# Performance work log

Measured on AMD Instinct MI355X. Metric: run time of the kernel, lower is better.

Reference implementation:

```python
import jax, jax.numpy as jnp
import numpy as np

B, L, K = 4, 1024, 48
EF, NF, NPE, NRBF, NCLS = 128, 128, 16, 16, 3
MAXREL = 32
EDGE_IN = NPE + NRBF * 25  # 416


def setup_inputs():
    key = jax.random.key(0)
    ks = jax.random.split(key, 8)
    X = jax.random.normal(ks[0], (B, L, 4, 3), jnp.float32)
    mask = jnp.ones((B, L), jnp.float32)
    R_idx = jnp.arange(B * L, dtype=jnp.int64).reshape(B, L)
    chain_labels = jax.random.randint(ks[1], (B, L), 0, 4).astype(jnp.int64)
    membrane_per_residue_labels = jax.random.randint(ks[2], (B, L), 0, NCLS).astype(jnp.int64)
    pe_w = jax.random.normal(ks[3], (2 * MAXREL + 2, NPE), jnp.float32) * 0.05
    pe_b = jax.random.normal(ks[4], (NPE,), jnp.float32) * 0.05
    edge_w = jax.random.normal(ks[5], (EDGE_IN, EF), jnp.float32) * 0.05
    ne_g = jnp.ones((EF,), jnp.float32)
    ne_b = jnp.zeros((EF,), jnp.float32)
    node_w = jax.random.normal(ks[6], (NCLS, NF), jnp.float32) * 0.05
    nn_g = jnp.ones((NF,), jnp.float32)
    nn_b = jnp.zeros((NF,), jnp.float32)
    return {"X": X, "mask": mask, "R_idx": R_idx, "chain_labels": chain_labels,
            "membrane_per_residue_labels": membrane_per_residue_labels,
            "pe_w": pe_w, "pe_b": pe_b, "edge_w": edge_w, "ne_g": ne_g, "ne_b": ne_b,
            "node_w": node_w, "nn_g": nn_g, "nn_b": nn_b}


def _rbf(D):
    mu = jnp.linspace(2.0, 22.0, NRBF)
    sigma = (22.0 - 2.0) / NRBF
    return jnp.exp(-(((D[..., None] - mu) / sigma) ** 2))


def _gather_nb(v, e_idx):
    # v: [B, L, ...] -> [B, L, K, ...] gathered along residue dim
    return jax.vmap(lambda vi, ii: vi[ii])(v, e_idx)


def _ln(x, g, b, eps=1e-5):
    mu = jnp.mean(x, -1, keepdims=True)
    var = jnp.mean((x - mu) ** 2, -1, keepdims=True)
    return (x - mu) / jnp.sqrt(var + eps) * g + b


# 24 atom-pair RBFs after the Ca-Ca (D_neighbors) one, in the original concat order
PAIRS = [("N","N"),("C","C"),("O","O"),("Cb","Cb"),("Ca","N"),("Ca","C"),("Ca","O"),
         ("Ca","Cb"),("N","C"),("N","O"),("N","Cb"),("Cb","C"),("Cb","O"),("O","C"),
         ("N","Ca"),("C","Ca"),("O","Ca"),("Cb","Ca"),("C","N"),("O","N"),("Cb","N"),
         ("C","Cb"),("O","Cb"),("C","O")]


def reference(X, mask, R_idx, chain_labels, membrane_per_residue_labels,
              pe_w, pe_b, edge_w, ne_g, ne_b, node_w, nn_g, nn_b):
    Na, Ca, Cc, Oo = X[:, :, 0], X[:, :, 1], X[:, :, 2], X[:, :, 3]
    bvec = Ca - Na
    cvec = Cc - Ca
    avec = jnp.cross(bvec, cvec)
    Cb = -0.58273431 * avec + 0.56802827 * bvec - 0.54067466 * cvec + Ca
    coords = {"N": Na, "Ca": Ca, "C": Cc, "O": Oo, "Cb": Cb}

    # masked Ca-Ca distances + kNN (single NxN pass)
    mask2 = mask[:, :, None] * mask[:, None, :]
    dX = Ca[:, :, None, :] - Ca[:, None, :, :]
    D = mask2 * jnp.sqrt(jnp.sum(dX ** 2, -1) + 1e-6)
    D_max = jnp.max(D, -1, keepdims=True)
    D_adj = D + (1.0 - mask2) * D_max
    negD, E_idx = jax.lax.top_k(-D_adj, K)
    D_neighbors = -negD  # [B, L, K]

    # gather neighbor coords once, compute the 25 RBF features on N*K pairs only
    nb = {n: _gather_nb(v, E_idx) for n, v in coords.items()}  # [B, L, K, 3]
    rbf_list = [_rbf(D_neighbors)]
    for an, bn in PAIRS:
        d = jnp.sqrt(jnp.sum((coords[an][:, :, None, :] - nb[bn]) ** 2, -1) + 1e-6)
        rbf_list.append(_rbf(d))
    RBF_all = jnp.concatenate(rbf_list, -1)  # [B, L, K, 400]

    # positional encodings on gathered offsets / chain equality
    off = R_idx[:, :, None] - _gather_nb(R_idx, E_idx)           # [B, L, K]
    E_chains = (chain_labels[:, :, None] == _gather_nb(chain_labels, E_idx)).astype(jnp.int32)
    d = jnp.clip(off + MAXREL, 0, 2 * MAXREL).astype(jnp.int32) * E_chains + (1 - E_chains) * (2 * MAXREL + 1)
    d1h = jax.nn.one_hot(d, 2 * MAXREL + 2, dtype=jnp.float32)
    E_pos = d1h @ pe_w + pe_b                                     # [B, L, K, 16]

    E = jnp.concatenate([E_pos, RBF_all], -1) @ edge_w            # [B, L, K, 128]
    E = _ln(E, ne_g, ne_b)

    C1h = jax.nn.one_hot(membrane_per_residue_labels, NCLS, dtype=jnp.float32)
    V = _ln(C1h @ node_w, nn_g, nn_b)                             # [B, L, 128]
    return V, E, E_idx
```

## Files before the change

kernel.cpp:

```cpp
#include <hip/hip_runtime.h>
#include <math.h>

#define B_ 4
#define L_ 1024
#define K_ 48
#define EF_ 128
#define NF_ 128
#define NPE_ 16
#define NRBF_ 16
#define MAXREL_ 32
#define EDGE_IN_ 416

#define V_SIZE   (B_*L_*NF_)
#define E_OFF    (V_SIZE)
#define E_SIZE   (B_*L_*K_*EF_)
#define EIDX_OFF (E_OFF + E_SIZE)

#define XH_STRIDE 232
#define SE_STRIDE 132

typedef __attribute__((ext_vector_type(8))) short bf16x8;
typedef __attribute__((ext_vector_type(4))) float f32x4;
typedef __attribute__((ext_vector_type(4))) unsigned u32x4;

__device__ const int PA_[25] = {1, 0,2,3,4, 1,1,1,1, 0,0,0, 4,4, 3, 0,2,3,4, 2,3,4, 2,3, 2};
__device__ const int PB_[25] = {1, 0,2,3,4, 0,2,3,4, 2,3,4, 2,3, 2, 1,1,1,1, 0,0,0, 4,4, 3};

__device__ __forceinline__ unsigned short f2bf(float f){
    unsigned u = __float_as_uint(f);
    unsigned r = u + 0x7fffu + ((u >> 16) & 1u);
    return (unsigned short)(r >> 16);
}

__global__ __launch_bounds__(256) void wprep_kernel(const float* __restrict__ w,
                                                    unsigned short* __restrict__ wt)
{
    int idx = blockIdx.x * 256 + threadIdx.x;
    if (idx >= EDGE_IN_ * EF_) return;
    int f = idx & 127;
    int k = idx >> 7;
    wt[f * EDGE_IN_ + k] = f2bf(w[k * EF_ + f]);
}

__global__ __launch_bounds__(128) void v_kernel(const int* __restrict__ labels,
                                                const float* __restrict__ node_w,
                                                const float* __restrict__ g,
                                                const float* __restrict__ bb,
                                                float* __restrict__ out)
{
    int gi = blockIdx.x;
    int f  = threadIdx.x;
    int lbl = labels[gi];
    float v = node_w[lbl*NF_ + f];

    __shared__ float red[2];
    __shared__ float red2[2];
    float s = v;
    #pragma unroll
    for (int m = 1; m < 64; m <<= 1) s += __shfl_xor(s, m, 64);
    if ((f & 63) == 0) red[f >> 6] = s;
    __syncthreads();
    float mu = (red[0] + red[1]) * (1.0f / NF_);
    float d = v - mu;
    float s2 = d * d;
    #pragma unroll
    for (int m = 1; m < 64; m <<= 1) s2 += __shfl_xor(s2, m, 64);
    if ((f & 63) == 0) red2[f >> 6] = s2;
    __syncthreads();
    float var = (red2[0] + red2[1]) * (1.0f / NF_);
    out[gi*NF_ + f] = d * rsqrtf(var + 1e-5f) * g[f] + bb[f];
}

__global__ __launch_bounds__(256, 5) void fused_kernel(const float* __restrict__ X,
                                                   const float* __restrict__ mask,
                                                   const int* __restrict__ Ridx,
                                                   const int* __restrict__ chains,
                                                   const float* __restrict__ pe_w,
                                                   const float* __restrict__ pe_b,
                                                   const unsigned short* __restrict__ wt,
                                                   const float* __restrict__ ne_g,
                                                   const float* __restrict__ ne_b,
                                                   float* __restrict__ out)
{
    __shared__ __align__(16) unsigned char sBuf[K_ * SE_STRIDE * 4];
    float* sCa = (float*)sBuf;
    float* sM  = (float*)(sBuf + 12288);
    unsigned short* xh = (unsigned short*)sBuf;
    float* sE = (float*)sBuf;

    __shared__ float sAI[16];
    __shared__ float sAJ[K_][16];
    __shared__ int   sJ[K_];
    __shared__ int   sDpos[K_];
    __shared__ unsigned hist[256];
    __shared__ float wmax[4];
    __shared__ int sSelBin;
    __shared__ unsigned sSelLo, sSelCnt;
    __shared__ unsigned long long sTkey;
    __shared__ unsigned long long cand[K_];
    __shared__ unsigned sCnt;

    int tid = threadIdx.x;
    int gi  = blockIdx.x;
    int b   = gi >> 10;
    int i   = gi & (L_ - 1);

    for (int idx = tid; idx < L_ * 3; idx += 256) {
        int j = idx / 3, d = idx - j * 3;
        sCa[idx] = X[(((size_t)((b << 10) + j)) * 4 + 1) * 3 + d];
    }
    for (int j = tid; j < L_; j += 256) sM[j] = mask[(b << 10) + j];
    if (tid == 0) sCnt = 0;
    __syncthreads();

    float cx = sCa[i*3+0], cy = sCa[i*3+1], cz = sCa[i*3+2];
    float mi = sM[i];

    float lmax = 0.0f;
    #pragma unroll
    for (int q = 0; q < 4; ++q) {
        int j = tid + q * 256;
        float dx = cx - sCa[j*3+0];
        float dy = cy - sCa[j*3+1];
        float dz = cz - sCa[j*3+2];
        float dist = sqrtf(dx*dx + dy*dy + dz*dz + 1e-6f);
        lmax = fmaxf(lmax, mi * sM[j] * dist);
    }
    #pragma unroll
    for (int m = 1; m < 64; m <<= 1) lmax = fmaxf(lmax, __shfl_xor(lmax, m, 64));
    if ((tid & 63) == 0) wmax[tid >> 6] = lmax;
    __syncthreads();
    float Dmax = fmaxf(fmaxf(wmax[0], wmax[1]), fmaxf(wmax[2], wmax[3]));

    unsigned long long key[4];
    bool act[4];
    #pragma unroll
    for (int q = 0; q < 4; ++q) {
        int j = tid + q * 256;
        float dx = cx - sCa[j*3+0];
        float dy = cy - sCa[j*3+1];
        float dz = cz - sCa[j*3+2];
        float dist = sqrtf(dx*dx + dy*dy + dz*dz + 1e-6f);
        float m2 = mi * sM[j];
        float Dadj = m2 * dist + (1.0f - m2) * Dmax;
        key[q] = (((unsigned long long)__float_as_uint(Dadj)) << 32) | (unsigned)j;
        act[q] = true;
    }

    unsigned r = K_ - 1;
    unsigned long long T = 0;
    const int shifts[6] = {56, 48, 40, 32, 8, 0};
    #pragma unroll 1
    for (int p = 0; p < 6; ++p) {
        int sh = shifts[p];
        hist[tid] = 0;
        __syncthreads();
        #pragma unroll
        for (int q = 0; q < 4; ++q)
            if (act[q]) atomicAdd(&hist[(unsigned)((key[q] >> sh) & 255ULL)], 1u);
        __syncthreads();
        if (tid < 64) {
            unsigned b0 = hist[tid*4+0], b1 = hist[tid*4+1], b2 = hist[tid*4+2], b3 = hist[tid*4+3];
            unsigned s0 = b0, s1 = s0 + b1, s2 = s1 + b2, s3 = s2 + b3;
            unsigned s = s3;
            #pragma unroll
            for (int m = 1; m < 64; m <<= 1) {
                unsigned o = __shfl_up(s, m, 64);
                if (tid >= m) s += o;
            }
            unsigned base = s - s3;
            hist[tid*4+0] = base + s0;
            hist[tid*4+1] = base + s1;
            hist[tid*4+2] = base + s2;
            hist[tid*4+3] = base + s3;
        }
        __syncthreads();
        unsigned lo = (tid == 0) ? 0u : hist[tid - 1];
        unsigned hi = hist[tid];
        if (r >= lo && r < hi) { sSelBin = tid; sSelLo = lo; sSelCnt = hi - lo; }
        __syncthreads();
        int bsel = sSelBin;
        r -= sSelLo;
        T |= ((unsigned long long)(unsigned)bsel) << sh;
        #pragma unroll
        for (int q = 0; q < 4; ++q)
            act[q] = act[q] && ((unsigned)((key[q] >> sh) & 255ULL) == (unsigned)bsel);
        if (sSelCnt == 1) {
            #pragma unroll
            for (int q = 0; q < 4; ++q)
                if (act[q]) sTkey = key[q];
            __syncthreads();
            T = sTkey;
            break;
        }
        __syncthreads();
    }

    #pragma unroll
    for (int q = 0; q < 4; ++q)
        if (key[q] <= T) {
            unsigned pos = atomicAdd(&sCnt, 1u);
            cand[pos] = key[q];
        }
    __syncthreads();

    if (tid < 64) {
        unsigned long long k64 = (tid < K_) ? cand[tid] : 0xffffffffffffffffULL;
        #pragma unroll
        for (unsigned kk = 2; kk <= 64; kk <<= 1) {
            #pragma unroll
            for (unsigned jj = kk >> 1; jj > 0; jj >>= 1) {
                unsigned long long o = __shfl_xor(k64, jj, 64);
                bool lower = (tid & jj) == 0;
                bool asc   = (tid & kk) == 0;
                unsigned long long mn = (k64 < o) ? k64 : o;
                unsigned long long mx = (k64 < o) ? o : k64;
                k64 = (lower == asc) ? mn : mx;
            }
        }
        if (tid < K_) {
            int j = (int)(unsigned)(k64 & 0xffffffffULL);
            sJ[tid] = j;
            out[EIDX_OFF + (size_t)gi * K_ + tid] = (float)j;
        }
    }
    __syncthreads();

    if (tid < K_ + 1) {
        int rr = (tid < K_) ? sJ[tid] : i;
        const float* xr = X + ((size_t)((b << 10) + rr)) * 12;
        float n0=xr[0],  n1=xr[1],  n2=xr[2];
        float a0=xr[3],  a1=xr[4],  a2=xr[5];
        float c0=xr[6],  c1=xr[7],  c2=xr[8];
        float o0=xr[9],  o1=xr[10], o2=xr[11];
        float bx=a0-n0, by=a1-n1, bz=a2-n2;
        float vx=c0-a0, vy=c1-a1, vz=c2-a2;
        float ax = by*vz - bz*vy;
        float ay = bz*vx - bx*vz;
        float az = bx*vy - by*vx;
        float cb0 = -0.58273431f*ax + 0.56802827f*bx - 0.54067466f*vx + a0;
        float cb1 = -0.58273431f*ay + 0.56802827f*by - 0.54067466f*vy + a1;
        float cb2 = -0.58273431f*az + 0.56802827f*bz - 0.54067466f*vz + a2;
        float* dst = (tid < K_) ? &sAJ[tid][0] : &sAI[0];
        dst[0]=n0;  dst[1]=n1;  dst[2]=n2;
        dst[3]=a0;  dst[4]=a1;  dst[5]=a2;
        dst[6]=c0;  dst[7]=c1;  dst[8]=c2;
        dst[9]=o0;  dst[10]=o1; dst[11]=o2;
        dst[12]=cb0; dst[13]=cb1; dst[14]=cb2;
    }
    if (tid >= 64 && tid < 64 + K_) {
        int e = tid - 64;
        int j = sJ[e];
        int off  = Ridx[gi] - Ridx[(b << 10) + j];
        int same = (chains[gi] == chains[(b << 10) + j]);
        int dcl = off + MAXREL_;
        dcl = dcl < 0 ? 0 : (dcl > 2*MAXREL_ ? 2*MAXREL_ : dcl);
        sDpos[e] = same ? dcl : (2*MAXREL_ + 1);
    }
    __syncthreads();

    const int wv = tid >> 6;
    const int ln = tid & 63;
    const int lr = ln & 15;
    const int lg = ln >> 4;

    f32x4 acc[3][2];
    #pragma unroll
    for (int rf = 0; rf < 3; ++rf)
        #pragma unroll
        for (int cf = 0; cf < 2; ++cf)
            acc[rf][cf] = (f32x4){0.0f, 0.0f, 0.0f, 0.0f};

    const unsigned short* wbase0 = wt + (size_t)(wv*32 + lr) * EDGE_IN_ + lg*8;
    const unsigned short* wbase1 = wt + (size_t)(wv*32 + 16 + lr) * EDGE_IN_ + lg*8;

    #pragma unroll
    for (int h = 0; h < 2; ++h) {
        if (h == 0) {
            #pragma unroll
            for (int p = 0; p < 2; ++p) {
                int idx = tid + p * 256;
                if (idx < 384) {
                    int e = idx >> 3, cc = (idx & 7) * 2;
                    int dp = sDpos[e];
                    float v0 = pe_w[dp*NPE_ + cc]     + pe_b[cc];
                    float v1 = pe_w[dp*NPE_ + cc + 1] + pe_b[cc + 1];
                    unsigned pk;
                    asm("v_cvt_pk_bf16_f32 %0, %1, %2" : "=v"(pk) : "v"(v0), "v"(v1));
                    *(unsigned*)&xh[e * XH_STRIDE + cc] = pk;
                }
            }
            #pragma unroll
            for (int p = 0; p < 3; ++p) {
                int idx = tid + p * 256;
                if (idx < 624) {
                    int e = idx / 13, g2 = idx - e * 13;
                    float dx = sAI[PA_[g2]*3+0] - sAJ[e][PB_[g2]*3+0];
                    float dy = sAI[PA_[g2]*3+1] - sAJ[e][PB_[g2]*3+1];
                    float dz = sAI[PA_[g2]*3+2] - sAJ[e][PB_[g2]*3+2];
                    float dist = sqrtf(dx*dx + dy*dy + dz*dz + 1e-6f);
                    float t = 0.8f * dist - 1.6f;
                    unsigned pk[8];
                    #pragma unroll
                    for (int rr = 0; rr < 8; ++rr) {
                        float v0 = __expf(-t * t); t -= 1.06666672f;
                        float v1 = __expf(-t * t); t -= 1.06666672f;
                        asm("v_cvt_pk_bf16_f32 %0, %1, %2" : "=v"(pk[rr]) : "v"(v0), "v"(v1));
                    }
                    u32x4 w0 = {pk[0], pk[1], pk[2], pk[3]};
                    u32x4 w1 = {pk[4], pk[5], pk[6], pk[7]};
                    int cb = NPE_ + g2 * 16;
                    *(u32x4*)&xh[e * XH_STRIDE + cb]     = w0;
                    *(u32x4*)&xh[e * XH_STRIDE + cb + 8] = w1;
                }
            }
        } else {
            #pragma unroll
            for (int p = 0; p < 3; ++p) {
                int idx = tid + p * 256;
                if (idx < 576) {
                    int e = idx / 12, g2 = 13 + (idx - e * 12);
                    float dx = sAI[PA_[g2]*3+0] - sAJ[e][PB_[g2]*3+0];
                    float dy = sAI[PA_[g2]*3+1] - sAJ[e][PB_[g2]*3+1];
                    float dz = sAI[PA_[g2]*3+2] - sAJ[e][PB_[g2]*3+2];
                    float dist = sqrtf(dx*dx + dy*dy + dz*dz + 1e-6f);
                    float t = 0.8f * dist - 1.6f;
                    unsigned pk[8];
                    #pragma unroll
                    for (int rr = 0; rr < 8; ++rr) {
                        float v0 = __expf(-t * t); t -= 1.06666672f;
                        float v1 = __expf(-t * t); t -= 1.06666672f;
                        asm("v_cvt_pk_bf16_f32 %0, %1, %2" : "=v"(pk[rr]) : "v"(v0), "v"(v1));
                    }
                    u32x4 w0 = {pk[0], pk[1], pk[2], pk[3]};
                    u32x4 w1 = {pk[4], pk[5], pk[6], pk[7]};
                    int cb = (g2 - 13) * 16;
                    *(u32x4*)&xh[e * XH_STRIDE + cb]     = w0;
                    *(u32x4*)&xh[e * XH_STRIDE + cb + 8] = w1;
                }
            }
        }
        __syncthreads();

        const int kb  = h ? 224 : 0;
        const int nks = h ? 6 : 7;
        #pragma unroll 4
        for (int ks = 0; ks < nks; ++ks) {
            int k0 = ks * 32;
            bf16x8 a[3], bh[2];
            bh[0] = *(const bf16x8*)(wbase0 + kb + k0);
            bh[1] = *(const bf16x8*)(wbase1 + kb + k0);
            #pragma unroll
            for (int rf = 0; rf < 3; ++rf)
                a[rf] = *(const bf16x8*)&xh[(rf*16 + lr) * XH_STRIDE + k0 + lg*8];
            #pragma unroll
            for (int rf = 0; rf < 3; ++rf) {
                #pragma unroll
                for (int cf = 0; cf < 2; ++cf)
                    acc[rf][cf] = __builtin_amdgcn_mfma_f32_16x16x32_bf16(a[rf], bh[cf], acc[rf][cf], 0, 0, 0);
            }
        }
        __syncthreads();
    }

    #pragma unroll
    for (int rf = 0; rf < 3; ++rf)
        #pragma unroll
        for (int cf = 0; cf < 2; ++cf)
            #pragma unroll
            for (int r4 = 0; r4 < 4; ++r4) {
                int row = rf*16 + lg*4 + r4;
                int col = wv*32 + cf*16 + lr;
                sE[row * SE_STRIDE + col] = acc[rf][cf][r4];
            }
    __syncthreads();

    int l16 = tid & 15;
    float gv[8], bv[8];
    #pragma unroll
    for (int q = 0; q < 8; ++q) { gv[q] = ne_g[l16*8 + q]; bv[q] = ne_b[l16*8 + q]; }

    for (int p = 0; p < 3; ++p) {
        int e = p*16 + (tid >> 4);
        float vals[8];
        #pragma unroll
        for (int q = 0; q < 8; ++q) vals[q] = sE[e * SE_STRIDE + l16*8 + q];
        float sum = 0.0f;
        #pragma unroll
        for (int q = 0; q < 8; ++q) sum += vals[q];
        #pragma unroll
        for (int m = 1; m < 16; m <<= 1) sum += __shfl_xor(sum, m, 64);
        float mu = sum * (1.0f / 128.0f);
        float s2 = 0.0f;
        #pragma unroll
        for (int q = 0; q < 8; ++q) { float d = vals[q] - mu; s2 += d * d; }
        #pragma unroll
        for (int m = 1; m < 16; m <<= 1) s2 += __shfl_xor(s2, m, 64);
        float rstd = rsqrtf(s2 * (1.0f / 128.0f) + 1e-5f);

        float* dst = out + E_OFF + (size_t)(gi * K_ + e) * EF_ + l16*8;
        f32x4 o0, o1;
        o0[0] = (vals[0] - mu) * rstd * gv[0] + bv[0];
        o0[1] = (vals[1] - mu) * rstd * gv[1] + bv[1];
        o0[2] = (vals[2] - mu) * rstd * gv[2] + bv[2];
        o0[3] = (vals[3] - mu) * rstd * gv[3] + bv[3];
        o1[0] = (vals[4] - mu) * rstd * gv[4] + bv[4];
        o1[1] = (vals[5] - mu) * rstd * gv[5] + bv[5];
        o1[2] = (vals[6] - mu) * rstd * gv[6] + bv[6];
        o1[3] = (vals[7] - mu) * rstd * gv[7] + bv[7];
        __builtin_nontemporal_store(o0, (f32x4*)dst);
        __builtin_nontemporal_store(o1, (f32x4*)(dst + 4));
    }
}

extern "C" void kernel_launch(void* const* d_in, const int* in_sizes, int n_in,
                              void* d_out, int out_size, void* d_ws, size_t ws_size,
                              hipStream_t stream)
{
    const float* X      = (const float*)d_in[0];
    const float* mask   = (const float*)d_in[1];
    const int*   Ridx   = (const int*)d_in[2];
    const int*   chains = (const int*)d_in[3];
    const int*   memb   = (const int*)d_in[4];
    const float* pe_w   = (const float*)d_in[5];
    const float* pe_b   = (const float*)d_in[6];
    const float* edge_w = (const float*)d_in[7];
    const float* ne_g   = (const float*)d_in[8];
    const float* ne_b   = (const float*)d_in[9];
    const float* node_w = (const float*)d_in[10];
    const float* nn_g   = (const float*)d_in[11];
    const float* nn_b   = (const float*)d_in[12];
    float* out = (float*)d_out;

    unsigned short* wt = (unsigned short*)d_ws;

    wprep_kernel<<<(EDGE_IN_*EF_ + 255)/256, 256, 0, stream>>>(edge_w, wt);
    v_kernel<<<B_*L_, 128, 0, stream>>>(memb, node_w, nn_g, nn_b, out);
    fused_kernel<<<B_*L_, 256, 0, stream>>>(X, mask, Ridx, chains, pe_w, pe_b,
                                            wt, ne_g, ne_b, out);
}
```

Before: 97.85 us.

## Shrink LDS via quarter-sized feature staging and register-side LayerNorm

The bf16 feature tile is built and consumed in four K-chunks with a 136-element stride instead of two halves, so the shared buffer shrinks to 16KB. Scratch arrays are overlaid in one aux buffer, and launch bounds are raised to 7 blocks per SM. LayerNorm now runs straight from the MFMA accumulators using per-wave partial sums and a one-pass variance, with no fp32 staging of E in shared memory. The radix-select early exit is dropped and the first distance pass is reused. Costs: more barriers, scalar (non-vectorised) output stores, and a one-pass variance that is less numerically robust.

```diff
diff --git a/kernel.cpp b/kernel.cpp
--- a/kernel.cpp
+++ b/kernel.cpp
@@ -16,8 +16,7 @@
 #define E_SIZE   (B_*L_*K_*EF_)
 #define EIDX_OFF (E_OFF + E_SIZE)
 
-#define XH_STRIDE 232
-#define SE_STRIDE 132
+#define XH4_STRIDE 136
 
 typedef __attribute__((ext_vector_type(8))) short bf16x8;
 typedef __attribute__((ext_vector_type(4))) float f32x4;
@@ -30,6 +29,59 @@
     unsigned u = __float_as_uint(f);
     unsigned r = u + 0x7fffu + ((u >> 16) & 1u);
     return (unsigned short)(r >> 16);
+}
+
+__device__ __forceinline__ float pair_dist(const float* sAI, const float (*sAJ)[16], int e, int g2) {
+    float dx = sAI[PA_[g2]*3+0] - sAJ[e][PB_[g2]*3+0];
+    float dy = sAI[PA_[g2]*3+1] - sAJ[e][PB_[g2]*3+1];
+    float dz = sAI[PA_[g2]*3+2] - sAJ[e][PB_[g2]*3+2];
+    return sqrtf(dx*dx + dy*dy + dz*dz + 1e-6f);
+}
+
+__device__ __forceinline__ void rbf16(unsigned short* dst, float dist) {
+    float t = 0.8f * dist - 1.6f;
+    unsigned pk[8];
+    #pragma unroll
+    for (int rr = 0; rr < 8; ++rr) {
+        float v0 = __expf(-t * t); t -= 1.06666672f;
+        float v1 = __expf(-t * t); t -= 1.06666672f;
+        asm("v_cvt_pk_bf16_f32 %0, %1, %2" : "=v"(pk[rr]) : "v"(v0), "v"(v1));
+    }
+    u32x4 w0 = {pk[0], pk[1], pk[2], pk[3]};
+    u32x4 w1 = {pk[4], pk[5], pk[6], pk[7]};
+    *(u32x4*)dst = w0;
+    *(u32x4*)(dst + 8) = w1;
+}
+
+template<int NG, int GF, int CB>
+__device__ __forceinline__ void rbf_quarter(unsigned short* xh, const float* sAI,
+                                            const float (*sAJ)[16], int tid) {
+    for (int idx = tid; idx < K_ * NG; idx += 256) {
+        int e = idx / NG, g = idx - e * NG;
+        rbf16(&xh[e * XH4_STRIDE + CB + g * 16], pair_dist(sAI, sAJ, e, GF + g));
+    }
+}
+
+template<int NKS, int KB>
+__device__ __forceinline__ void mfma_quarter(f32x4 (&acc)[3][2], const unsigned short* xh,
+                                             const unsigned short* w0p, const unsigned short* w1p,
+                                             int lr, int lg) {
+    #pragma unroll
+    for (int ks = 0; ks < NKS; ++ks) {
+        int k0 = ks * 32;
+        bf16x8 a0, a1, a2, wb0, wb1;
+        wb0 = *(const bf16x8*)(w0p + KB + k0);
+        wb1 = *(const bf16x8*)(w1p + KB + k0);
+        a0 = *(const bf16x8*)&xh[(lr)      * XH4_STRIDE + k0 + lg*8];
+        a1 = *(const bf16x8*)&xh[(16 + lr) * XH4_STRIDE + k0 + lg*8];
+        a2 = *(const bf16x8*)&xh[(32 + lr) * XH4_STRIDE + k0 + lg*8];
+        acc[0][0] = __builtin_amdgcn_mfma_f32_16x16x32_bf16(a0, wb0, acc[0][0], 0, 0, 0);
+        acc[0][1] = __builtin_amdgcn_mfma_f32_16x16x32_bf16(a0, wb1, acc[0][1], 0, 0, 0);
+        acc[1][0] = __builtin_amdgcn_mfma_f32_16x16x32_bf16(a1, wb0, acc[1][0], 0, 0, 0);
+        acc[1][1] = __builtin_amdgcn_mfma_f32_16x16x32_bf16(a1, wb1, acc[1][1], 0, 0, 0);
+        acc[2][0] = __builtin_amdgcn_mfma_f32_16x16x32_bf16(a2, wb0, acc[2][0], 0, 0, 0);
+        acc[2][1] = __builtin_amdgcn_mfma_f32_16x16x32_bf16(a2, wb1, acc[2][1], 0, 0, 0);
+    }
 }
 
 __global__ __launch_bounds__(256) void wprep_kernel(const float* __restrict__ w,
@@ -71,7 +123,7 @@
     out[gi*NF_ + f] = d * rsqrtf(var + 1e-5f) * g[f] + bb[f];
 }
 
-__global__ __launch_bounds__(256, 5) void fused_kernel(const float* __restrict__ X,
+__global__ __launch_bounds__(256, 7) void fused_kernel(const float* __restrict__ X,
                                                    const float* __restrict__ mask,
                                                    const int* __restrict__ Ridx,
                                                    const int* __restrict__ chains,
@@ -82,23 +134,25 @@
                                                    const float* __restrict__ ne_b,
                                                    float* __restrict__ out)
 {
-    __shared__ __align__(16) unsigned char sBuf[K_ * SE_STRIDE * 4];
-    float* sCa = (float*)sBuf;
-    float* sM  = (float*)(sBuf + 12288);
-    unsigned short* xh = (unsigned short*)sBuf;
-    float* sE = (float*)sBuf;
-
+    __shared__ __align__(16) unsigned char sBuf[16384];
+    __shared__ __align__(16) unsigned char sAux[1536];
     __shared__ float sAI[16];
     __shared__ float sAJ[K_][16];
     __shared__ int   sJ[K_];
     __shared__ int   sDpos[K_];
-    __shared__ unsigned hist[256];
-    __shared__ float wmax[4];
-    __shared__ int sSelBin;
-    __shared__ unsigned sSelLo, sSelCnt;
-    __shared__ unsigned long long sTkey;
-    __shared__ unsigned long long cand[K_];
-    __shared__ unsigned sCnt;
+
+    float* sCa = (float*)sBuf;
+    float* sM  = (float*)(sBuf + 12288);
+    unsigned short* xh = (unsigned short*)sBuf;
+
+    unsigned long long* cand = (unsigned long long*)sAux;
+    unsigned* hist   = (unsigned*)(sAux + 384);
+    float*    wmax   = (float*)(sAux + 1408);
+    int*      sSelBin= (int*)(sAux + 1424);
+    unsigned* sSelLo = (unsigned*)(sAux + 1428);
+    unsigned* sCnt   = (unsigned*)(sAux + 1432);
+    float* stats  = (float*)sAux;
+    float* stats2 = (float*)(sAux + 768);
 
     int tid = threadIdx.x;
     int gi  = blockIdx.x;
@@ -110,30 +164,14 @@
         sCa[idx] = X[(((size_t)((b << 10) + j)) * 4 + 1) * 3 + d];
     }
     for (int j = tid; j < L_; j += 256) sM[j] = mask[(b << 10) + j];
-    if (tid == 0) sCnt = 0;
+    if (tid == 0) *sCnt = 0;
     __syncthreads();
 
     float cx = sCa[i*3+0], cy = sCa[i*3+1], cz = sCa[i*3+2];
     float mi = sM[i];
 
+    float dist4[4], m2r[4];
     float lmax = 0.0f;
-    #pragma unroll
-    for (int q = 0; q < 4; ++q) {
-        int j = tid + q * 256;
-        float dx = cx - sCa[j*3+0];
-        float dy = cy - sCa[j*3+1];
-        float dz = cz - sCa[j*3+2];
-        float dist = sqrtf(dx*dx + dy*dy + dz*dz + 1e-6f);
-        lmax = fmaxf(lmax, mi * sM[j] * dist);
-    }
-    #pragma unroll
-    for (int m = 1; m < 64; m <<= 1) lmax = fmaxf(lmax, __shfl_xor(lmax, m, 64));
-    if ((tid & 63) == 0) wmax[tid >> 6] = lmax;
-    __syncthreads();
-    float Dmax = fmaxf(fmaxf(wmax[0], wmax[1]), fmaxf(wmax[2], wmax[3]));
-
-    unsigned long long key[4];
-    bool act[4];
     #pragma unroll
     for (int q = 0; q < 4; ++q) {
         int j = tid + q * 256;
@@ -142,7 +180,21 @@
         float dz = cz - sCa[j*3+2];
         float dist = sqrtf(dx*dx + dy*dy + dz*dz + 1e-6f);
         float m2 = mi * sM[j];
-        float Dadj = m2 * dist + (1.0f - m2) * Dmax;
+        dist4[q] = dist; m2r[q] = m2;
+        lmax = fmaxf(lmax, m2 * dist);
+    }
+    #pragma unroll
+    for (int m = 1; m < 64; m <<= 1) lmax = fmaxf(lmax, __shfl_xor(lmax, m, 64));
+    if ((tid & 63) == 0) wmax[tid >> 6] = lmax;
+    __syncthreads();
+    float Dmax = fmaxf(fmaxf(wmax[0], wmax[1]), fmaxf(wmax[2], wmax[3]));
+
+    unsigned long long key[4];
+    bool act[4];
+    #pragma unroll
+    for (int q = 0; q < 4; ++q) {
+        int j = tid + q * 256;
+        float Dadj = m2r[q] * dist4[q] + (1.0f - m2r[q]) * Dmax;
         key[q] = (((unsigned long long)__float_as_uint(Dadj)) << 32) | (unsigned)j;
         act[q] = true;
     }
@@ -177,29 +229,21 @@
         __syncthreads();
         unsigned lo = (tid == 0) ? 0u : hist[tid - 1];
         unsigned hi = hist[tid];
-        if (r >= lo && r < hi) { sSelBin = tid; sSelLo = lo; sSelCnt = hi - lo; }
+        if (r >= lo && r < hi) { *sSelBin = tid; *sSelLo = lo; }
         __syncthreads();
-        int bsel = sSelBin;
-        r -= sSelLo;
+        int bsel = *sSelBin;
+        r -= *sSelLo;
         T |= ((unsigned long long)(unsigned)bsel) << sh;
         #pragma unroll
         for (int q = 0; q < 4; ++q)
             act[q] = act[q] && ((unsigned)((key[q] >> sh) & 255ULL) == (unsigned)bsel);
-        if (sSelCnt == 1) {
-            #pragma unroll
-            for (int q = 0; q < 4; ++q)
-                if (act[q]) sTkey = key[q];
-            __syncthreads();
-            T = sTkey;
-            break;
-        }
         __syncthreads();
     }
 
     #pragma unroll
     for (int q = 0; q < 4; ++q)
         if (key[q] <= T) {
-            unsigned pos = atomicAdd(&sCnt, 1u);
+            unsigned pos = atomicAdd(sCnt, 1u);
             cand[pos] = key[q];
         }
     __syncthreads();
@@ -275,142 +319,72 @@
     const unsigned short* wbase1 = wt + (size_t)(wv*32 + 16 + lr) * EDGE_IN_ + lg*8;
 
     #pragma unroll
-    for (int h = 0; h < 2; ++h) {
-        if (h == 0) {
+    for (int p = 0; p < 2; ++p) {
+        int idx = tid + p * 256;
+        if (idx < 384) {
+            int e = idx >> 3, cc = (idx & 7) * 2;
+            int dp = sDpos[e];
+            float v0 = pe_w[dp*NPE_ + cc]     + pe_b[cc];
+            float v1 = pe_w[dp*NPE_ + cc + 1] + pe_b[cc + 1];
+            unsigned pk;
+            asm("v_cvt_pk_bf16_f32 %0, %1, %2" : "=v"(pk) : "v"(v0), "v"(v1));
+            *(unsigned*)&xh[e * XH4_STRIDE + cc] = pk;
+        }
+    }
+    rbf_quarter<7, 0, 16>(xh, sAI, sAJ, tid);
+    __syncthreads();
+    mfma_quarter<4, 0>(acc, xh, wbase0, wbase1, lr, lg);
+    __syncthreads();
+    rbf_quarter<6, 7, 0>(xh, sAI, sAJ, tid);
+    __syncthreads();
+    mfma_quarter<3, 128>(acc, xh, wbase0, wbase1, lr, lg);
+    __syncthreads();
+    rbf_quarter<6, 13, 0>(xh, sAI, sAJ, tid);
+    __syncthreads();
+    mfma_quarter<3, 224>(acc, xh, wbase0, wbase1, lr, lg);
+    __syncthreads();
+    rbf_quarter<6, 19, 0>(xh, sAI, sAJ, tid);
+    __syncthreads();
+    mfma_quarter<3, 320>(acc, xh, wbase0, wbase1, lr, lg);
+
+    #pragma unroll
+    for (int rf = 0; rf < 3; ++rf)
+        #pragma unroll
+        for (int r4 = 0; r4 < 4; ++r4) {
+            float v0 = acc[rf][0][r4], v1 = acc[rf][1][r4];
+            float s  = v0 + v1;
+            float s2 = v0*v0 + v1*v1;
             #pragma unroll
-            for (int p = 0; p < 2; ++p) {
-                int idx = tid + p * 256;
-                if (idx < 384) {
-                    int e = idx >> 3, cc = (idx & 7) * 2;
-                    int dp = sDpos[e];
-                    float v0 = pe_w[dp*NPE_ + cc]     + pe_b[cc];
-                    float v1 = pe_w[dp*NPE_ + cc + 1] + pe_b[cc + 1];
-                    unsigned pk;
-                    asm("v_cvt_pk_bf16_f32 %0, %1, %2" : "=v"(pk) : "v"(v0), "v"(v1));
-                    *(unsigned*)&xh[e * XH_STRIDE + cc] = pk;
-                }
+            for (int m = 1; m < 16; m <<= 1) {
+                s  += __shfl_xor(s,  m, 64);
+                s2 += __shfl_xor(s2, m, 64);
             }
-            #pragma unroll
-            for (int p = 0; p < 3; ++p) {
-                int idx = tid + p * 256;
-                if (idx < 624) {
-                    int e = idx / 13, g2 = idx - e * 13;
-                    float dx = sAI[PA_[g2]*3+0] - sAJ[e][PB_[g2]*3+0];
-                    float dy = sAI[PA_[g2]*3+1] - sAJ[e][PB_[g2]*3+1];
-                    float dz = sAI[PA_[g2]*3+2] - sAJ[e][PB_[g2]*3+2];
-                    float dist = sqrtf(dx*dx + dy*dy + dz*dz + 1e-6f);
-                    float t = 0.8f * dist - 1.6f;
-                    unsigned pk[8];
-                    #pragma unroll
-                    for (int rr = 0; rr < 8; ++rr) {
-                        float v0 = __expf(-t * t); t -= 1.06666672f;
-                        float v1 = __expf(-t * t); t -= 1.06666672f;
-                        asm("v_cvt_pk_bf16_f32 %0, %1, %2" : "=v"(pk[rr]) : "v"(v0), "v"(v1));
-                    }
-                    u32x4 w0 = {pk[0], pk[1], pk[2], pk[3]};
-                    u32x4 w1 = {pk[4], pk[5], pk[6], pk[7]};
-                    int cb = NPE_ + g2 * 16;
-                    *(u32x4*)&xh[e * XH_STRIDE + cb]     = w0;
-                    *(u32x4*)&xh[e * XH_STRIDE + cb + 8] = w1;
-                }
+            if (lr == 0) {
+                int row = rf*16 + lg*4 + r4;
+                stats [wv*K_ + row] = s;
+                stats2[wv*K_ + row] = s2;
             }
-        } else {
-            #pragma unroll
-            for (int p = 0; p < 3; ++p) {
-                int idx = tid + p * 256;
-                if (idx < 576) {
-                    int e = idx / 12, g2 = 13 + (idx - e * 12);
-                    float dx = sAI[PA_[g2]*3+0] - sAJ[e][PB_[g2]*3+0];
-                    float dy = sAI[PA_[g2]*3+1] - sAJ[e][PB_[g2]*3+1];
-                    float dz = sAI[PA_[g2]*3+2] - sAJ[e][PB_[g2]*3+2];
-                    float dist = sqrtf(dx*dx + dy*dy + dz*dz + 1e-6f);
-                    float t = 0.8f * dist - 1.6f;
-                    unsigned pk[8];
-                    #pragma unroll
-                    for (int rr = 0; rr < 8; ++rr) {
-                        float v0 = __expf(-t * t); t -= 1.06666672f;
-                        float v1 = __expf(-t * t); t -= 1.06666672f;
-                        asm("v_cvt_pk_bf16_f32 %0, %1, %2" : "=v"(pk[rr]) : "v"(v0), "v"(v1));
-                    }
-                    u32x4 w0 = {pk[0], pk[1], pk[2], pk[3]};
-                    u32x4 w1 = {pk[4], pk[5], pk[6], pk[7]};
-                    int cb = (g2 - 13) * 16;
-                    *(u32x4*)&xh[e * XH_STRIDE + cb]     = w0;
-                    *(u32x4*)&xh[e * XH_STRIDE + cb + 8] = w1;
-                }
-            }
-        }
-        __syncthreads();
-
-        const int kb  = h ? 224 : 0;
-        const int nks = h ? 6 : 7;
-        #pragma unroll 4
-        for (int ks = 0; ks < nks; ++ks) {
-            int k0 = ks * 32;
-            bf16x8 a[3], bh[2];
-            bh[0] = *(const bf16x8*)(wbase0 + kb + k0);
-            bh[1] = *(const bf16x8*)(wbase1 + kb + k0);
-            #pragma unroll
-            for (int rf = 0; rf < 3; ++rf)
-                a[rf] = *(const bf16x8*)&xh[(rf*16 + lr) * XH_STRIDE + k0 + lg*8];
-            #pragma unroll
-            for (int rf = 0; rf < 3; ++rf) {
-                #pragma unroll
-                for (int cf = 0; cf < 2; ++cf)
-                    acc[rf][cf] = __builtin_amdgcn_mfma_f32_16x16x32_bf16(a[rf], bh[cf], acc[rf][cf], 0, 0, 0);
-            }
-        }
-        __syncthreads();
-    }
+        }
+    __syncthreads();
+
+    int colg = wv*32 + lr;
+    float gv0 = ne_g[colg],      bv0 = ne_b[colg];
+    float gv1 = ne_g[colg + 16], bv1 = ne_b[colg + 16];
 
     #pragma unroll
     for (int rf = 0; rf < 3; ++rf)
         #pragma unroll
-        for (int cf = 0; cf < 2; ++cf)
-            #pragma unroll
-            for (int r4 = 0; r4 < 4; ++r4) {
-                int row = rf*16 + lg*4 + r4;
-                int col = wv*32 + cf*16 + lr;
-                sE[row * SE_STRIDE + col] = acc[rf][cf][r4];
-            }
-    __syncthreads();
-
-    int l16 = tid & 15;
-    float gv[8], bv[8];
-    #pragma unroll
-    for (int q = 0; q < 8; ++q) { gv[q] = ne_g[l16*8 + q]; bv[q] = ne_b[l16*8 + q]; }
-
-    for (int p = 0; p < 3; ++p) {
-        int e = p*16 + (tid >> 4);
-        float vals[8];
-        #pragma unroll
-        for (int q = 0; q < 8; ++q) vals[q] = sE[e * SE_STRIDE + l16*8 + q];
-        float sum = 0.0f;
-        #pragma unroll
-        for (int q = 0; q < 8; ++q) sum += vals[q];
-        #pragma unroll
-        for (int m = 1; m < 16; m <<= 1) sum += __shfl_xor(sum, m, 64);
-        float mu = sum * (1.0f / 128.0f);
-        float s2 = 0.0f;
-        #pragma unroll
-        for (int q = 0; q < 8; ++q) { float d = vals[q] - mu; s2 += d * d; }
-        #pragma unroll
-        for (int m = 1; m < 16; m <<= 1) s2 += __shfl_xor(s2, m, 64);
-        float rstd = rsqrtf(s2 * (1.0f / 128.0f) + 1e-5f);
-
-        float* dst = out + E_OFF + (size_t)(gi * K_ + e) * EF_ + l16*8;
-        f32x4 o0, o1;
-        o0[0] = (vals[0] - mu) * rstd * gv[0] + bv[0];
-        o0[1] = (vals[1] - mu) * rstd * gv[1] + bv[1];
-        o0[2] = (vals[2] - mu) * rstd * gv[2] + bv[2];
-        o0[3] = (vals[3] - mu) * rstd * gv[3] + bv[3];
-        o1[0] = (vals[4] - mu) * rstd * gv[4] + bv[4];
-        o1[1] = (vals[5] - mu) * rstd * gv[5] + bv[5];
-        o1[2] = (vals[6] - mu) * rstd * gv[6] + bv[6];
-        o1[3] = (vals[7] - mu) * rstd * gv[7] + bv[7];
-        __builtin_nontemporal_store(o0, (f32x4*)dst);
-        __builtin_nontemporal_store(o1, (f32x4*)(dst + 4));
-    }
+        for (int r4 = 0; r4 < 4; ++r4) {
+            int row = rf*16 + lg*4 + r4;
+            float sum = stats [row] + stats [K_ + row] + stats [2*K_ + row] + stats [3*K_ + row];
+            float sq  = stats2[row] + stats2[K_ + row] + stats2[2*K_ + row] + stats2[3*K_ + row];
+            float mu   = sum * (1.0f / 128.0f);
+            float var  = sq * (1.0f / 128.0f) - mu * mu;
+            float rstd = rsqrtf(var + 1e-5f);
+            float* dst = out + E_OFF + (size_t)(gi * K_ + row) * EF_ + colg;
+            __builtin_nontemporal_store((acc[rf][0][r4] - mu) * rstd * gv0 + bv0, dst);
+            __builtin_nontemporal_store((acc[rf][1][r4] - mu) * rstd * gv1 + bv1, dst + 16);
+        }
 }
 
 extern "C" void kernel_launch(void* const* d_in, const int* in_sizes, int n_in,
```

Measured after the change: 110.0 us. 1.12x slower.
